# Optimization experiments

Hardware: AMD Instinct MI355X
Metric: run time of the kernel (lower is better)

The kernel has to match this reference:

```python
import jax, jax.numpy as jnp
import numpy as np

N_NODES = 100000
N_EDGES = 1600000
IN_DIM = 256
OUT_DIM = 64


def setup_inputs() -> dict:
    key = jax.random.key(0)
    k1, k2, k3, k4, k5 = jax.random.split(key, 5)
    h = jax.random.normal(k1, (N_NODES, IN_DIM), dtype=jnp.float32)
    src = jax.random.randint(k2, (N_EDGES,), 0, N_NODES, dtype=jnp.int32)
    dst = jax.random.randint(k3, (N_EDGES,), 0, N_NODES, dtype=jnp.int32)
    # xavier_normal with gain for relu (sqrt(2))
    gain = float(np.sqrt(2.0))
    std_w = gain * float(np.sqrt(2.0 / (IN_DIM + OUT_DIM)))
    W = jax.random.normal(k4, (OUT_DIM, IN_DIM), dtype=jnp.float32) * std_w
    std_a = gain * float(np.sqrt(2.0 / (2 * OUT_DIM + 1)))
    a = jax.random.normal(k5, (2 * OUT_DIM,), dtype=jnp.float32) * std_a
    return {"h": h, "src": src, "dst": dst, "W": W, "a": a}


def reference(h, src, dst, W, a):
    # linear projection: W_h[n, out]
    W_h = h @ W.T
    # edge attention: e = relu(a . concat(W_h[src], W_h[dst]))
    a_src, a_dst = a[:OUT_DIM], a[OUT_DIM:]
    e = jax.nn.relu(W_h[src] @ a_src + W_h[dst] @ a_dst)  # [E]
    # segment softmax over incoming edges of each dst node
    m = jax.ops.segment_max(e, dst, num_segments=N_NODES)  # [N]
    ex = jnp.exp(e - m[dst])
    s = jax.ops.segment_sum(ex, dst, num_segments=N_NODES)  # [N]
    alpha = ex / s[dst]  # [E]
    # weighted scatter-sum of source messages
    h_N = jax.ops.segment_sum(alpha[:, None] * W_h[src], dst, num_segments=N_NODES)
    return h_N
```

## Files before the change

kernel.cpp:

```cpp
#include <hip/hip_runtime.h>
#include <hip/hip_bf16.h>
#include <math.h>
#include <stdint.h>

#define N_NODES 100000
#define N_EDGES 1600000
#define IN_DIM 256
#define OUT_DIM 64

#define CWIN  64
#define NCB   1563
#define NPART 256
#define EPP   (N_EDGES / NPART)
#define SCAN_N (NCB * NPART)
#define SCAN_BLK ((SCAN_N + 4095) / 4096)
#define MAXE  1536

#define GEMM_BLKS ((N_NODES + 255) / 256)


typedef __attribute__((ext_vector_type(8))) short bh8;
typedef __attribute__((ext_vector_type(4))) float f4;

typedef __attribute__((address_space(1))) const void GV;
typedef __attribute__((address_space(3))) void LV;

static __device__ __forceinline__ unsigned short f2bf(float f) {
    unsigned u = __float_as_uint(f);
    unsigned r = (u + 0x7FFFu + ((u >> 16) & 1u)) >> 16;
    return (unsigned short)r;
}

__global__ __launch_bounds__(1024) void gat_hist_wprep(
    const int* __restrict__ dst, int* __restrict__ cur2dT,
    const float* __restrict__ W, unsigned short* __restrict__ WB)
{
    const int t = threadIdx.x;

    if (blockIdx.x >= NPART) {
        const int cell = (blockIdx.x - NPART) * 1024 + t;
        const int cl = cell & 15;
        const int nt = (cell >> 4) & 3;
        const int k16 = cell >> 6;
        const int col = nt * 16 + cl;
        const float4 lo = *(const float4*)(W + col * IN_DIM + k16 * 8);
        const float4 hi = *(const float4*)(W + col * IN_DIM + k16 * 8 + 4);
        unsigned short tmp[8];
        tmp[0] = f2bf(lo.x); tmp[1] = f2bf(lo.y);
        tmp[2] = f2bf(lo.z); tmp[3] = f2bf(lo.w);
        tmp[4] = f2bf(hi.x); tmp[5] = f2bf(hi.y);
        tmp[6] = f2bf(hi.z); tmp[7] = f2bf(hi.w);
        *(uint4*)&WB[(size_t)cell * 8] = *(uint4*)tmp;
        return;
    }

    __shared__ int lh[NCB];
    for (int i = t; i < NCB; i += 1024) lh[i] = 0;
    __syncthreads();
    const int e0 = blockIdx.x * EPP;
    for (int e = e0 + t; e < e0 + EPP; e += 1024)
        atomicAdd(&lh[dst[e] >> 6], 1);
    __syncthreads();
    for (int i = t; i < NCB; i += 1024)
        cur2dT[blockIdx.x * NCB + i] = lh[i];
}

__global__ __launch_bounds__(1024) void gat_scan1(int* __restrict__ data,
                                                  int* __restrict__ bsum)
{
    __shared__ int ts[1024];
    const int Lbase = blockIdx.x * 4096 + threadIdx.x * 4;
    int v[4], S[4];
    #pragma unroll
    for (int j = 0; j < 4; ++j) {
        const int L = Lbase + j;
        S[j] = (L & 255) * NCB + (L >> 8);
        v[j] = (L < SCAN_N) ? data[S[j]] : 0;
    }
    const int tsum = v[0] + v[1] + v[2] + v[3];
    ts[threadIdx.x] = tsum;
    __syncthreads();
    int val = tsum;
    for (int s = 1; s < 1024; s <<= 1) {
        const int add = (threadIdx.x >= s) ? ts[threadIdx.x - s] : 0;
        __syncthreads();
        val += add;
        ts[threadIdx.x] = val;
        __syncthreads();
    }
    int run = val - tsum;
    #pragma unroll
    for (int j = 0; j < 4; ++j) {
        const int L = Lbase + j;
        if (L < SCAN_N) data[S[j]] = run;
        run += v[j];
    }
    if (threadIdx.x == 1023) bsum[blockIdx.x] = val;
}

#define INLINE_BSUM_PREFIX(pbs, w0s)                                          \
{                                                                             \
    if (threadIdx.x < 128) {                                                  \
        const int v_ = (threadIdx.x < SCAN_BLK) ? bsum[threadIdx.x] : 0;      \
        int val_ = v_;                                                        \
        _Pragma("unroll")                                                     \
        for (int s_ = 1; s_ < 64; s_ <<= 1) {                                 \
            const int n_ = __shfl_up(val_, s_);                               \
            if ((threadIdx.x & 63) >= s_) val_ += n_;                         \
        }                                                                     \
        if (threadIdx.x == 63) w0s = val_;                                    \
        pbs[threadIdx.x] = val_ - v_;                                         \
    }                                                                         \
    __syncthreads();                                                          \
    if (threadIdx.x >= 64 && threadIdx.x < 128) pbs[threadIdx.x] += w0s;      \
    __syncthreads();                                                          \
}

__global__ __launch_bounds__(1024) void gat_gemm_scatter(
    const float* __restrict__ h, const unsigned short* __restrict__ WB,
    const float* __restrict__ a, unsigned short* __restrict__ WhB,
    float* __restrict__ p_src, float* __restrict__ p_dst,
    const int* __restrict__ src, const int* __restrict__ dst,
    const int* __restrict__ cur2dT, const int* __restrict__ bsum,
    int* __restrict__ ebufA)
{
    __shared__ __align__(16) unsigned short Wlds[64 * 256];
    __shared__ int pbs[128];
    __shared__ int w0s;

    const int t = threadIdx.x;

    if (blockIdx.x >= GEMM_BLKS) {
        const int part = blockIdx.x - GEMM_BLKS;
        int* lcur = (int*)Wlds;

        INLINE_BSUM_PREFIX(pbs, w0s)

        for (int i = t; i < NCB; i += 1024) {
            const int L = i * NPART + part;
            lcur[i] = cur2dT[part * NCB + i] + pbs[L >> 12];
        }
        __syncthreads();
        const int e0 = part * EPP;
        for (int e = e0 + t; e < e0 + EPP; e += 1024) {
            const int se = src[e], de = dst[e];
            const int pos = atomicAdd(&lcur[de >> 6], 1);
            ebufA[pos] = se | ((de & (CWIN - 1)) << 17);
        }
        return;
    }

    const int lane = t & 63;
    const int wv = t >> 6;
    const int cl = lane & 15;
    const int g  = lane >> 4;
    const int node0 = blockIdx.x * 256 + wv * 16;

    {
        #pragma unroll
        for (int i = 0; i < 2; ++i) {
            const int chunk = wv * 2 + i;
            __builtin_amdgcn_global_load_lds(
                (GV*)(WB + chunk * 512 + lane * 8),
                (LV*)(((char*)Wlds) + chunk * 1024), 16, 0, 0);
        }
    }
    __syncthreads();

    int row = node0 + cl;
    row = (row < N_NODES) ? row : N_NODES - 1;
    const float* __restrict__ hp = h + (size_t)row * IN_DIM + g * 8;

    f4 acc[4];
    #pragma unroll
    for (int nt = 0; nt < 4; ++nt) acc[nt] = (f4){0.f, 0.f, 0.f, 0.f};

    #pragma unroll
    for (int j = 0; j < 8; ++j) {
        const float4 lo = *(const float4*)(hp + j * 32);
        const float4 hi = *(const float4*)(hp + j * 32 + 4);
        bh8 af;
        af[0] = (short)f2bf(lo.x); af[1] = (short)f2bf(lo.y);
        af[2] = (short)f2bf(lo.z); af[3] = (short)f2bf(lo.w);
        af[4] = (short)f2bf(hi.x); af[5] = (short)f2bf(hi.y);
        af[6] = (short)f2bf(hi.z); af[7] = (short)f2bf(hi.w);

        #pragma unroll
        for (int nt = 0; nt < 4; ++nt) {
            const bh8 bf = *(const bh8*)&Wlds[(((j * 4 + g) * 64) + nt * 16 + cl) * 8];
            acc[nt] = __builtin_amdgcn_mfma_f32_16x16x32_bf16(af, bf, acc[nt], 0, 0, 0);
        }
    }

    float aS[4], aD[4];
    #pragma unroll
    for (int nt = 0; nt < 4; ++nt) {
        aS[nt] = a[nt * 16 + cl];
        aD[nt] = a[OUT_DIM + nt * 16 + cl];
    }

    #pragma unroll
    for (int r = 0; r < 4; ++r) {
        const int orow = node0 + g * 4 + r;
        float ps = 0.f, pd = 0.f;
        #pragma unroll
        for (int nt = 0; nt < 4; ++nt) {
            ps = fmaf(acc[nt][r], aS[nt], ps);
            pd = fmaf(acc[nt][r], aD[nt], pd);
        }
        #pragma unroll
        for (int o = 8; o > 0; o >>= 1) {
            ps += __shfl_xor(ps, o);
            pd += __shfl_xor(pd, o);
        }
        if (orow < N_NODES) {
            const unsigned lo2 = (unsigned)f2bf(acc[0][r]) |
                                 ((unsigned)f2bf(acc[1][r]) << 16);
            const unsigned hi2 = (unsigned)f2bf(acc[2][r]) |
                                 ((unsigned)f2bf(acc[3][r]) << 16);
            *(uint2*)&WhB[(size_t)orow * OUT_DIM + cl * 4] = make_uint2(lo2, hi2);
            if (cl == 0) { p_src[orow] = ps; p_dst[orow] = pd; }
        }
    }
}

__global__ __launch_bounds__(256) void gat_agg_fused(
    const int* __restrict__ ebufA, const int* __restrict__ cur2dT,
    const int* __restrict__ bsum,
    const float* __restrict__ p_src, const float* __restrict__ p_dst,
    const unsigned short* __restrict__ Wh, float* __restrict__ out)
{
    __shared__ int2 ledge[MAXE];
    __shared__ int lhist[CWIN], lbase[CWIN];
    __shared__ float pdl[CWIN];
    __shared__ int pbs[128];
    __shared__ int w0s;

    const int t = threadIdx.x;
    const int cb = blockIdx.x;

    INLINE_BSUM_PREFIX(pbs, w0s)

    const int a0 = cur2dT[cb] + pbs[cb >> 4];
    int a1 = N_EDGES;
    if (cb < NCB - 1) a1 = cur2dT[cb + 1] + pbs[(cb + 1) >> 4];
    const int cnt = min(a1 - a0, MAXE);
    const int wbase = cb * CWIN;

    if (t < CWIN) {
        lhist[t] = 0;
        const int node = wbase + t;
        pdl[t] = (node < N_NODES) ? p_dst[node] : 0.f;
    }
    __syncthreads();

    int   ev[6], rk[6];
    float ps[6];
    #pragma unroll
    for (int j = 0; j < 6; ++j) {
        const int i = t + j * 256;
        ev[j] = 0; rk[j] = 0; ps[j] = 0.f;
        if (i < cnt) {
            const int e = ebufA[a0 + i];
            ev[j] = e;
            ps[j] = p_src[e & 0x1FFFF];
            rk[j] = atomicAdd(&lhist[(e >> 17) & (CWIN - 1)], 1);
        }
    }
    __syncthreads();

    if (t < 64) {
        const int own = lhist[t];
        int val = own;
        #pragma unroll
        for (int s = 1; s < 64; s <<= 1) {
            const int n = __shfl_up(val, s);
            if (t >= s) val += n;
        }
        lbase[t] = val - own;
    }
    __syncthreads();

    #pragma unroll
    for (int j = 0; j < 6; ++j) {
        const int i = t + j * 256;
        if (i < cnt) {
            const int e = ev[j];
            const int ln = (e >> 17) & (CWIN - 1);
            const float ex = __expf(fmaxf(ps[j] + pdl[ln], 0.f));
            ledge[lbase[ln] + rk[j]] = make_int2(e & 0x1FFFF, __float_as_int(ex));
        }
    }
    __syncthreads();

    const int lane = t & 63;
    const int wv = t >> 6;
    const int grp = lane >> 4;
    const int ci = lane & 15;
    const int c4 = ci * 4;

    #pragma unroll
    for (int rr = 0; rr < 4; ++rr) {
        const int ln = wv * 16 + rr * 4 + grp;
        const int node = wbase + ln;
        const int sb = lbase[ln];
        const int d  = (node < N_NODES) ? lhist[ln] : 0;

        float ssum = 0.f;
        float a0f = 0.f, a1f = 0.f, a2f = 0.f, a3f = 0.f;

        #pragma unroll 4
        for (int k = 0; k < d; ++k) {
            const int2 ed = ledge[sb + k];
            const float ex = __int_as_float(ed.y);
            const uint2 wr = *(const uint2*)(Wh + (size_t)ed.x * OUT_DIM + c4);
            ssum += ex;
            a0f = fmaf(ex, __uint_as_float(wr.x << 16), a0f);
            a1f = fmaf(ex, __uint_as_float(wr.x & 0xFFFF0000u), a1f);
            a2f = fmaf(ex, __uint_as_float(wr.y << 16), a2f);
            a3f = fmaf(ex, __uint_as_float(wr.y & 0xFFFF0000u), a3f);
        }

        if (node < N_NODES) {
            const float inv = (d > 0) ? 1.f / ssum : 0.f;
            float* ob = out + (size_t)node * OUT_DIM;
            ob[ci]      = a0f * inv;
            ob[16 + ci] = a1f * inv;
            ob[32 + ci] = a2f * inv;
            ob[48 + ci] = a3f * inv;
        }
    }
}

extern "C" void kernel_launch(void* const* d_in, const int* in_sizes, int n_in,
                              void* d_out, int out_size, void* d_ws, size_t ws_size,
                              hipStream_t stream)
{
    const float* h  = (const float*)d_in[0];
    const int* src  = (const int*)d_in[1];
    const int* dst  = (const int*)d_in[2];
    const float* W  = (const float*)d_in[3];
    const float* a  = (const float*)d_in[4];
    float* out = (float*)d_out;

    char* ws = (char*)d_ws;
    unsigned short* WhB = (unsigned short*)(ws);
    float* p_src   = (float*)(ws + 12800000);
    float* p_dst   = (float*)(ws + 13200000);
    int*   cur2dT  = (int*)  (ws + 13600000);
    int*   bsum    = (int*)  (ws + 15200512);
    int*   ebufA   = (int*)  (ws + 15200904);
    unsigned short* WB = (unsigned short*)(ws + 21601024);

    gat_hist_wprep<<<NPART + 2, 1024, 0, stream>>>(dst, cur2dT, W, WB);
    gat_scan1<<<SCAN_BLK, 1024, 0, stream>>>(cur2dT, bsum);
    gat_gemm_scatter<<<GEMM_BLKS + NPART, 1024, 0, stream>>>(
        h, WB, a, WhB, p_src, p_dst, src, dst, cur2dT, bsum, ebufA);
    gat_agg_fused<<<NCB, 256, 0, stream>>>(ebufA, cur2dT, bsum, p_src, p_dst,
                                           WhB, out);
}
```

Baseline: 89.85 us.

## Replace histogram+scan bucketing with fixed-capacity per-window buckets and global atomics

Removes the separate histogram, scan and W-prep kernels. Each partition block now builds its local histogram, reserves slots in fixed-capacity per-window buckets through global atomics, and scatters edges in the same kernel as the GEMM. Each GEMM block converts W to bf16 straight into LDS. This cuts two kernel launches and the scan pass, at the cost of a memset, redundant W conversion in every GEMM block, and a padded edge buffer. Edge order within a bucket now depends on atomic timing, and windows holding more edges than the capacity are silently truncated.

```diff
diff --git a/kernel.cpp b/kernel.cpp
--- a/kernel.cpp
+++ b/kernel.cpp
@@ -12,9 +12,8 @@
 #define NCB   1563
 #define NPART 256
 #define EPP   (N_EDGES / NPART)
-#define SCAN_N (NCB * NPART)
-#define SCAN_BLK ((SCAN_N + 4095) / 4096)
-#define MAXE  1536
+#define EBCAP 1536
+#define MAXE  EBCAP
 
 #define GEMM_BLKS ((N_NODES + 255) / 256)
 
@@ -31,18 +30,53 @@
     return (unsigned short)r;
 }
 
-__global__ __launch_bounds__(1024) void gat_hist_wprep(
-    const int* __restrict__ dst, int* __restrict__ cur2dT,
-    const float* __restrict__ W, unsigned short* __restrict__ WB)
+__global__ __launch_bounds__(1024) void gat_mega(
+    const float* __restrict__ h, const float* __restrict__ W,
+    const float* __restrict__ a, unsigned short* __restrict__ WhB,
+    float* __restrict__ p_src, float* __restrict__ p_dst,
+    const int* __restrict__ src, const int* __restrict__ dst,
+    int* __restrict__ gcur, int* __restrict__ ebufA)
 {
+    __shared__ __align__(16) unsigned short Wlds[64 * 256];
+
     const int t = threadIdx.x;
 
-    if (blockIdx.x >= NPART) {
-        const int cell = (blockIdx.x - NPART) * 1024 + t;
-        const int cl = cell & 15;
-        const int nt = (cell >> 4) & 3;
+    if (blockIdx.x >= GEMM_BLKS) {
+        const int part = blockIdx.x - GEMM_BLKS;
+        int* lh   = (int*)Wlds;
+        int* lcur = ((int*)Wlds) + NCB;
+
+        for (int i = t; i < NCB; i += 1024) lh[i] = 0;
+        __syncthreads();
+        const int e0 = part * EPP;
+        for (int e = e0 + t; e < e0 + EPP; e += 1024)
+            atomicAdd(&lh[dst[e] >> 6], 1);
+        __syncthreads();
+        for (int i = t; i < NCB; i += 1024) {
+            const int c = lh[i];
+            lcur[i] = c ? atomicAdd(&gcur[i], c) : 0;
+        }
+        __syncthreads();
+        for (int e = e0 + t; e < e0 + EPP; e += 1024) {
+            const int se = src[e], de = dst[e];
+            const int w = de >> 6;
+            const int off = atomicAdd(&lcur[w], 1);
+            ebufA[w * EBCAP + off] = se | ((de & (CWIN - 1)) << 17);
+        }
+        return;
+    }
+
+    const int lane = t & 63;
+    const int wv = t >> 6;
+    const int cl = lane & 15;
+    const int g  = lane >> 4;
+    const int node0 = blockIdx.x * 256 + wv * 16;
+
+    #pragma unroll
+    for (int cc = 0; cc < 2; ++cc) {
+        const int cell = t + cc * 1024;
+        const int col = cell & 63;
         const int k16 = cell >> 6;
-        const int col = nt * 16 + cl;
         const float4 lo = *(const float4*)(W + col * IN_DIM + k16 * 8);
         const float4 hi = *(const float4*)(W + col * IN_DIM + k16 * 8 + 4);
         unsigned short tmp[8];
@@ -50,120 +84,7 @@
         tmp[2] = f2bf(lo.z); tmp[3] = f2bf(lo.w);
         tmp[4] = f2bf(hi.x); tmp[5] = f2bf(hi.y);
         tmp[6] = f2bf(hi.z); tmp[7] = f2bf(hi.w);
-        *(uint4*)&WB[(size_t)cell * 8] = *(uint4*)tmp;
-        return;
-    }
-
-    __shared__ int lh[NCB];
-    for (int i = t; i < NCB; i += 1024) lh[i] = 0;
-    __syncthreads();
-    const int e0 = blockIdx.x * EPP;
-    for (int e = e0 + t; e < e0 + EPP; e += 1024)
-        atomicAdd(&lh[dst[e] >> 6], 1);
-    __syncthreads();
-    for (int i = t; i < NCB; i += 1024)
-        cur2dT[blockIdx.x * NCB + i] = lh[i];
-}
-
-__global__ __launch_bounds__(1024) void gat_scan1(int* __restrict__ data,
-                                                  int* __restrict__ bsum)
-{
-    __shared__ int ts[1024];
-    const int Lbase = blockIdx.x * 4096 + threadIdx.x * 4;
-    int v[4], S[4];
-    #pragma unroll
-    for (int j = 0; j < 4; ++j) {
-        const int L = Lbase + j;
-        S[j] = (L & 255) * NCB + (L >> 8);
-        v[j] = (L < SCAN_N) ? data[S[j]] : 0;
-    }
-    const int tsum = v[0] + v[1] + v[2] + v[3];
-    ts[threadIdx.x] = tsum;
-    __syncthreads();
-    int val = tsum;
-    for (int s = 1; s < 1024; s <<= 1) {
-        const int add = (threadIdx.x >= s) ? ts[threadIdx.x - s] : 0;
-        __syncthreads();
-        val += add;
-        ts[threadIdx.x] = val;
-        __syncthreads();
-    }
-    int run = val - tsum;
-    #pragma unroll
-    for (int j = 0; j < 4; ++j) {
-        const int L = Lbase + j;
-        if (L < SCAN_N) data[S[j]] = run;
-        run += v[j];
-    }
-    if (threadIdx.x == 1023) bsum[blockIdx.x] = val;
-}
-
-#define INLINE_BSUM_PREFIX(pbs, w0s)                                          \
-{                                                                             \
-    if (threadIdx.x < 128) {                                                  \
-        const int v_ = (threadIdx.x < SCAN_BLK) ? bsum[threadIdx.x] : 0;      \
-        int val_ = v_;                                                        \
-        _Pragma("unroll")                                                     \
-        for (int s_ = 1; s_ < 64; s_ <<= 1) {                                 \
-            const int n_ = __shfl_up(val_, s_);                               \
-            if ((threadIdx.x & 63) >= s_) val_ += n_;                         \
-        }                                                                     \
-        if (threadIdx.x == 63) w0s = val_;                                    \
-        pbs[threadIdx.x] = val_ - v_;                                         \
-    }                                                                         \
-    __syncthreads();                                                          \
-    if (threadIdx.x >= 64 && threadIdx.x < 128) pbs[threadIdx.x] += w0s;      \
-    __syncthreads();                                                          \
-}
-
-__global__ __launch_bounds__(1024) void gat_gemm_scatter(
-    const float* __restrict__ h, const unsigned short* __restrict__ WB,
-    const float* __restrict__ a, unsigned short* __restrict__ WhB,
-    float* __restrict__ p_src, float* __restrict__ p_dst,
-    const int* __restrict__ src, const int* __restrict__ dst,
-    const int* __restrict__ cur2dT, const int* __restrict__ bsum,
-    int* __restrict__ ebufA)
-{
-    __shared__ __align__(16) unsigned short Wlds[64 * 256];
-    __shared__ int pbs[128];
-    __shared__ int w0s;
-
-    const int t = threadIdx.x;
-
-    if (blockIdx.x >= GEMM_BLKS) {
-        const int part = blockIdx.x - GEMM_BLKS;
-        int* lcur = (int*)Wlds;
-
-        INLINE_BSUM_PREFIX(pbs, w0s)
-
-        for (int i = t; i < NCB; i += 1024) {
-            const int L = i * NPART + part;
-            lcur[i] = cur2dT[part * NCB + i] + pbs[L >> 12];
-        }
-        __syncthreads();
-        const int e0 = part * EPP;
-        for (int e = e0 + t; e < e0 + EPP; e += 1024) {
-            const int se = src[e], de = dst[e];
-            const int pos = atomicAdd(&lcur[de >> 6], 1);
-            ebufA[pos] = se | ((de & (CWIN - 1)) << 17);
-        }
-        return;
-    }
-
-    const int lane = t & 63;
-    const int wv = t >> 6;
-    const int cl = lane & 15;
-    const int g  = lane >> 4;
-    const int node0 = blockIdx.x * 256 + wv * 16;
-
-    {
-        #pragma unroll
-        for (int i = 0; i < 2; ++i) {
-            const int chunk = wv * 2 + i;
-            __builtin_amdgcn_global_load_lds(
-                (GV*)(WB + chunk * 512 + lane * 8),
-                (LV*)(((char*)Wlds) + chunk * 1024), 16, 0, 0);
-        }
+        *(uint4*)&Wlds[cell * 8] = *(uint4*)tmp;
     }
     __syncthreads();
 
@@ -225,26 +146,18 @@
 }
 
 __global__ __launch_bounds__(256) void gat_agg_fused(
-    const int* __restrict__ ebufA, const int* __restrict__ cur2dT,
-    const int* __restrict__ bsum,
+    const int* __restrict__ ebufA, const int* __restrict__ gcnt,
     const float* __restrict__ p_src, const float* __restrict__ p_dst,
     const unsigned short* __restrict__ Wh, float* __restrict__ out)
 {
     __shared__ int2 ledge[MAXE];
     __shared__ int lhist[CWIN], lbase[CWIN];
     __shared__ float pdl[CWIN];
-    __shared__ int pbs[128];
-    __shared__ int w0s;
 
     const int t = threadIdx.x;
     const int cb = blockIdx.x;
-
-    INLINE_BSUM_PREFIX(pbs, w0s)
-
-    const int a0 = cur2dT[cb] + pbs[cb >> 4];
-    int a1 = N_EDGES;
-    if (cb < NCB - 1) a1 = cur2dT[cb + 1] + pbs[(cb + 1) >> 4];
-    const int cnt = min(a1 - a0, MAXE);
+    const int a0 = cb * EBCAP;
+    const int cnt = min(gcnt[cb], MAXE);
     const int wbase = cb * CWIN;
 
     if (t < CWIN) {
@@ -347,15 +260,11 @@
     unsigned short* WhB = (unsigned short*)(ws);
     float* p_src   = (float*)(ws + 12800000);
     float* p_dst   = (float*)(ws + 13200000);
-    int*   cur2dT  = (int*)  (ws + 13600000);
-    int*   bsum    = (int*)  (ws + 15200512);
-    int*   ebufA   = (int*)  (ws + 15200904);
-    unsigned short* WB = (unsigned short*)(ws + 21601024);
-
-    gat_hist_wprep<<<NPART + 2, 1024, 0, stream>>>(dst, cur2dT, W, WB);
-    gat_scan1<<<SCAN_BLK, 1024, 0, stream>>>(cur2dT, bsum);
-    gat_gemm_scatter<<<GEMM_BLKS + NPART, 1024, 0, stream>>>(
-        h, WB, a, WhB, p_src, p_dst, src, dst, cur2dT, bsum, ebufA);
-    gat_agg_fused<<<NCB, 256, 0, stream>>>(ebufA, cur2dT, bsum, p_src, p_dst,
-                                           WhB, out);
-}
+    int*   gcur    = (int*)  (ws + 13600000);
+    int*   ebufA   = (int*)  (ws + 13606252 + 4);
+
+    hipMemsetAsync(gcur, 0, NCB * sizeof(int), stream);
+    gat_mega<<<GEMM_BLKS + NPART, 1024, 0, stream>>>(
+        h, W, a, WhB, p_src, p_dst, src, dst, gcur, ebufA);
+    gat_agg_fused<<<NCB, 256, 0, stream>>>(ebufA, gcur, p_src, p_dst, WhB, out);
+}
```

Result: faster. 85.58 us (median of 2 runs) (-4.8%).
